# Performance work log

Hardware: AMD Instinct MI355X
Metric: run time of the kernel (lower is better)

Reference implementation:

```python
import jax, jax.numpy as jnp
import numpy as np


def setup_inputs() -> dict:
    key = jax.random.key(0)
    B, N = 4, 32768
    xyz = jax.random.normal(key, (B, N, 3), dtype=jnp.float32)
    return {"xyz": xyz, "K": 16, "nqueries": 2048}


def reference(xyz, K, nqueries):
    # xyz: (b, n, 3). Deterministic strided pick of nqueries query points
    # (stand-in for the KD-tree's distance-pick sampling), then brute-force KNN.
    b, n, _ = xyz.shape
    stride = n // nqueries
    q_idx = jnp.arange(nqueries) * stride          # (nq,)
    pts = xyz[:, q_idx, :]                          # (b, nq, 3) sampled query points
    # pairwise squared distances (b, nq, n)
    d = jnp.sum((pts[:, :, None, :] - xyz[:, None, :, :]) ** 2, axis=-1)
    _, idx = jax.lax.top_k(-d, K)                   # (b, nq, K) nearest-neighbor indices
    idx = idx.astype(jnp.int64)[..., None]          # (b, nq, K, 1) matches expand_dims(..., 3)
    return idx, pts
```

## Files before the change

### kernel.cpp

```cpp
#include <hip/hip_runtime.h>
#include <stdint.h>

#define NPTS  32768
#define NQ    2048
#define KNN   16
#define NB    4
#define BLOCK 256
#define WPB   4
#define PPL   8
#define ITERS (NPTS / (64 * PPL))
#define GATE_MARGIN 5e-4f

__device__ __forceinline__ int dpp_shr1_i(int x) {
    return __builtin_amdgcn_update_dpp(x, x, 0x111, 0xf, 0xf, false);
}
__device__ __forceinline__ float dpp_shr1_f(float x) {
    return __int_as_float(dpp_shr1_i(__float_as_int(x)));
}
__device__ __forceinline__ float readlane_f(float x, int l) {
    return __int_as_float(__builtin_amdgcn_readlane(__float_as_int(x), l));
}

template <int T>
__device__ __forceinline__ void insert_all(float d, int p, int lane,
                                           float& ld, int& li, float& tau,
                                           float& th, float qnm)
{
    unsigned long long rem = __ballot(d <= tau);
    while (rem) {
        const int srcl = __ffsll(rem) - 1;
        const float wd = readlane_f(d, srcl);
        const int   wi = __builtin_amdgcn_readlane(p, srcl);
        const bool less = (ld < wd) || (ld == wd && li < wi);
        const unsigned long long lm = __ballot(less);
        const int pos = __popc((unsigned)((lm >> (16 * T)) & 0xffffull));
        const float pld = dpp_shr1_f(ld);
        const int   pli = dpp_shr1_i(li);
        if ((lane >> 4) == T) {
            const int gl = lane & 15;
            if (gl == pos)      { ld = wd;  li = wi;  }
            else if (gl > pos)  { ld = pld; li = pli; }
        }
        tau = readlane_f(ld, 16 * T + 15);
        th  = tau + qnm;
        rem &= rem - 1;
        if (rem) rem &= __ballot(d <= tau);
    }
}

__device__ __forceinline__ void load6(float4 dst[6], const float4* p) {
    #pragma unroll
    for (int t = 0; t < 6; ++t) dst[t] = p[t];
}

__device__ __forceinline__ void step(const float4 c[6], int pb, int lane,
                                     float m2x0, float m2y0, float m2z0,
                                     float m2x1, float m2y1, float m2z1,
                                     float qx0, float qy0, float qz0,
                                     float qx1, float qy1, float qz1,
                                     float& ld, int& li,
                                     float& tau0, float& tau1,
                                     float& th0, float& th1,
                                     float qnm0, float qnm1)
{
    float px[PPL], py[PPL], pz[PPL];
    px[0] = c[0].x; py[0] = c[0].y; pz[0] = c[0].z;
    px[1] = c[0].w; py[1] = c[1].x; pz[1] = c[1].y;
    px[2] = c[1].z; py[2] = c[1].w; pz[2] = c[2].x;
    px[3] = c[2].y; py[3] = c[2].z; pz[3] = c[2].w;
    px[4] = c[3].x; py[4] = c[3].y; pz[4] = c[3].z;
    px[5] = c[3].w; py[5] = c[4].x; pz[5] = c[4].y;
    px[6] = c[4].z; py[6] = c[4].w; pz[6] = c[5].x;
    px[7] = c[5].y; py[7] = c[5].z; pz[7] = c[5].w;

    unsigned long long m0[PPL], m1[PPL], any = 0;
    #pragma unroll
    for (int j = 0; j < PPL; ++j) {
        const float s = __fmaf_rn(pz[j], pz[j],
                          __fmaf_rn(py[j], py[j], __fmul_rn(px[j], px[j])));
        float t0 = __fmaf_rn(px[j], m2x0, s);
        t0 = __fmaf_rn(py[j], m2y0, t0);
        t0 = __fmaf_rn(pz[j], m2z0, t0);
        m0[j] = __ballot(t0 <= th0);
        float t1 = __fmaf_rn(px[j], m2x1, s);
        t1 = __fmaf_rn(py[j], m2y1, t1);
        t1 = __fmaf_rn(pz[j], m2z1, t1);
        m1[j] = __ballot(t1 <= th1);
        any |= m0[j] | m1[j];
    }
    if (any) {
        #pragma unroll
        for (int j = 0; j < PPL; ++j) {
            if (m0[j]) {
                const float dx = __fadd_rn(px[j], -qx0);
                const float dy = __fadd_rn(py[j], -qy0);
                const float dz = __fadd_rn(pz[j], -qz0);
                const float d  = __fadd_rn(
                    __fadd_rn(__fmul_rn(dx, dx), __fmul_rn(dy, dy)),
                    __fmul_rn(dz, dz));
                insert_all<0>(d, pb + j, lane, ld, li, tau0, th0, qnm0);
            }
        }
        #pragma unroll
        for (int j = 0; j < PPL; ++j) {
            if (m1[j]) {
                const float dx = __fadd_rn(px[j], -qx1);
                const float dy = __fadd_rn(py[j], -qy1);
                const float dz = __fadd_rn(pz[j], -qz1);
                const float d  = __fadd_rn(
                    __fadd_rn(__fmul_rn(dx, dx), __fmul_rn(dy, dy)),
                    __fmul_rn(dz, dz));
                insert_all<1>(d, pb + j, lane, ld, li, tau1, th1, qnm1);
            }
        }
    }
}

__global__ __launch_bounds__(BLOCK) void knn_kernel(const float* __restrict__ xyz,
                                                    float* __restrict__ out_idx,
                                                    float* __restrict__ out_pts)
{
    const int tid  = threadIdx.x;
    const int lane = tid & 63;
    const int wv   = tid >> 6;
    const int w    = blockIdx.x * WPB + wv;
    const int b    = w >> 10;
    const int pr   = w & 1023;
    const size_t base = (size_t)b * NPTS * 3;

    const int qp0 = pr << 5;
    const float qx0 = xyz[base + 3 * qp0 + 0];
    const float qy0 = xyz[base + 3 * qp0 + 1];
    const float qz0 = xyz[base + 3 * qp0 + 2];
    const float qx1 = xyz[base + 3 * qp0 + 48];
    const float qy1 = xyz[base + 3 * qp0 + 49];
    const float qz1 = xyz[base + 3 * qp0 + 50];

    const int g0 = b * NQ + (pr << 1);
    if (lane == 0) {
        out_pts[3 * g0 + 0] = qx0;
        out_pts[3 * g0 + 1] = qy0;
        out_pts[3 * g0 + 2] = qz0;
        out_pts[3 * g0 + 3] = qx1;
        out_pts[3 * g0 + 4] = qy1;
        out_pts[3 * g0 + 5] = qz1;
    }

    const float m2x0 = -2.0f * qx0, m2y0 = -2.0f * qy0, m2z0 = -2.0f * qz0;
    const float m2x1 = -2.0f * qx1, m2y1 = -2.0f * qy1, m2z1 = -2.0f * qz1;
    const float qnm0 = -(qx0 * qx0 + qy0 * qy0 + qz0 * qz0) + GATE_MARGIN;
    const float qnm1 = -(qx1 * qx1 + qy1 * qy1 + qz1 * qz1) + GATE_MARGIN;

    float ld = __builtin_inff();  int li = 0x7fffffff;
    float tau0 = __builtin_inff(), tau1 = __builtin_inff();
    float th0  = __builtin_inff(), th1  = __builtin_inff();

    const float4* lp = (const float4*)(xyz + base) + 6 * lane;

    float4 A[6], Bf[6];
    load6(A, lp);
    for (int k = 0; k < ITERS; k += 2) {
        load6(Bf, lp + 384);
        step(A, (k << 9) + PPL * lane, lane,
             m2x0, m2y0, m2z0, m2x1, m2y1, m2z1,
             qx0, qy0, qz0, qx1, qy1, qz1,
             ld, li, tau0, tau1, th0, th1, qnm0, qnm1);
        if (k + 2 < ITERS)
            load6(A, lp + 768);
        step(Bf, ((k + 1) << 9) + PPL * lane, lane,
             m2x0, m2y0, m2z0, m2x1, m2y1, m2z1,
             qx0, qy0, qz0, qx1, qy1, qz1,
             ld, li, tau0, tau1, th0, th1, qnm0, qnm1);
        lp += 768;
    }

    if (lane < 2 * KNN) {
        out_idx[(size_t)g0 * KNN + lane] = (float)li;
    }
}

extern "C" void kernel_launch(void* const* d_in, const int* in_sizes, int n_in,
                              void* d_out, int out_size, void* d_ws, size_t ws_size,
                              hipStream_t stream) {
    const float* xyz = (const float*)d_in[0];
    float* out = (float*)d_out;
    float* out_idx = out;
    float* out_pts = out + (size_t)NB * NQ * KNN;

    const int blocks = (NB * NQ / 2) / WPB;
    knn_kernel<<<blocks, BLOCK, 0, stream>>>(xyz, out_idx, out_pts);
}
```

Measured before the change: 186.4 us.

## Repack points into float4 with precomputed norms and use one query per wave

Result: slower. 301.1 us (+61.5%).

```diff
diff --git a/kernel.cpp b/kernel.cpp
--- a/kernel.cpp
+++ b/kernel.cpp
@@ -5,10 +5,6 @@
 #define NQ    2048
 #define KNN   16
 #define NB    4
-#define BLOCK 256
-#define WPB   4
-#define PPL   8
-#define ITERS (NPTS / (64 * PPL))
 #define GATE_MARGIN 5e-4f
 
 __device__ __forceinline__ int dpp_shr1_i(int x) {
@@ -48,20 +44,133 @@
     }
 }
 
+__global__ __launch_bounds__(256) void repack_kernel(const float* __restrict__ xyz,
+                                                     float4* __restrict__ ws)
+{
+    const int i = blockIdx.x * 256 + threadIdx.x;
+    const float4* src = (const float4*)xyz + 3 * (size_t)i;
+    const float4 c0 = src[0], c1 = src[1], c2 = src[2];
+    float px[4], py[4], pz[4];
+    px[0] = c0.x; py[0] = c0.y; pz[0] = c0.z;
+    px[1] = c0.w; py[1] = c1.x; pz[1] = c1.y;
+    px[2] = c1.z; py[2] = c1.w; pz[2] = c2.x;
+    px[3] = c2.y; py[3] = c2.z; pz[3] = c2.w;
+    float4* dst = ws + 4 * (size_t)i;
+    #pragma unroll
+    for (int t = 0; t < 4; ++t) {
+        const float s = __fmaf_rn(pz[t], pz[t],
+                          __fmaf_rn(py[t], py[t], __fmul_rn(px[t], px[t])));
+        dst[t] = make_float4(px[t], py[t], pz[t], s);
+    }
+}
+
+#define BLOCKA 256
+#define WPBA   4
+#define PPLA   4
+#define ITERSA (NPTS / (64 * PPLA))
+
+__device__ __forceinline__ void load4(float4 dst[4], const float4* p) {
+    #pragma unroll
+    for (int t = 0; t < 4; ++t) dst[t] = p[t];
+}
+
+__device__ __forceinline__ void stepA(const float4 c[4], int pb, int lane,
+                                      float m2x, float m2y, float m2z,
+                                      float qx, float qy, float qz,
+                                      float& ld, int& li,
+                                      float& tau, float& th, float qnm)
+{
+    unsigned long long m[4], any = 0;
+    #pragma unroll
+    for (int j = 0; j < PPLA; ++j) {
+        float t = __fmaf_rn(c[j].x, m2x, c[j].w);
+        t = __fmaf_rn(c[j].y, m2y, t);
+        t = __fmaf_rn(c[j].z, m2z, t);
+        m[j] = __ballot(t <= th);
+        any |= m[j];
+    }
+    if (any) {
+        #pragma unroll
+        for (int j = 0; j < PPLA; ++j) {
+            if (m[j]) {
+                const float dx = __fadd_rn(c[j].x, -qx);
+                const float dy = __fadd_rn(c[j].y, -qy);
+                const float dz = __fadd_rn(c[j].z, -qz);
+                const float d  = __fadd_rn(
+                    __fadd_rn(__fmul_rn(dx, dx), __fmul_rn(dy, dy)),
+                    __fmul_rn(dz, dz));
+                insert_all<0>(d, pb + j, lane, ld, li, tau, th, qnm);
+            }
+        }
+    }
+}
+
+__global__ __launch_bounds__(BLOCKA) void knn1(const float4* __restrict__ wsp,
+                                               float* __restrict__ out_idx,
+                                               float* __restrict__ out_pts)
+{
+    const int tid  = threadIdx.x;
+    const int lane = tid & 63;
+    const int wv   = tid >> 6;
+    const int w    = blockIdx.x * WPBA + wv;
+    const int b    = w >> 11;
+    const int qi   = w & 2047;
+    const float4* pbase = wsp + (size_t)b * NPTS;
+
+    const float4 qv = pbase[qi << 4];
+    const float qx = qv.x, qy = qv.y, qz = qv.z;
+    const float m2x = -2.0f * qx, m2y = -2.0f * qy, m2z = -2.0f * qz;
+    const float qnm = -qv.w + GATE_MARGIN;
+
+    const int g = b * NQ + qi;
+    if (lane == 0) {
+        out_pts[3 * g + 0] = qx;
+        out_pts[3 * g + 1] = qy;
+        out_pts[3 * g + 2] = qz;
+    }
+
+    float ld = __builtin_inff();  int li = 0x7fffffff;
+    float tau = __builtin_inff(), th = __builtin_inff();
+
+    const float4* lp = pbase + 4 * lane;
+
+    float4 A[4], Bf[4];
+    load4(A, lp);
+    for (int k = 0; k < ITERSA; k += 2) {
+        load4(Bf, lp + 256);
+        stepA(A, (k << 8) + 4 * lane, lane, m2x, m2y, m2z,
+              qx, qy, qz, ld, li, tau, th, qnm);
+        if (k + 2 < ITERSA)
+            load4(A, lp + 512);
+        stepA(Bf, ((k + 1) << 8) + 4 * lane, lane, m2x, m2y, m2z,
+              qx, qy, qz, ld, li, tau, th, qnm);
+        lp += 512;
+    }
+
+    if (lane < KNN) {
+        out_idx[(size_t)g * KNN + lane] = (float)li;
+    }
+}
+
+#define BLOCK 256
+#define WPB   4
+#define PPL   8
+#define ITERS (NPTS / (64 * PPL))
+
 __device__ __forceinline__ void load6(float4 dst[6], const float4* p) {
     #pragma unroll
     for (int t = 0; t < 6; ++t) dst[t] = p[t];
 }
 
-__device__ __forceinline__ void step(const float4 c[6], int pb, int lane,
-                                     float m2x0, float m2y0, float m2z0,
-                                     float m2x1, float m2y1, float m2z1,
-                                     float qx0, float qy0, float qz0,
-                                     float qx1, float qy1, float qz1,
-                                     float& ld, int& li,
-                                     float& tau0, float& tau1,
-                                     float& th0, float& th1,
-                                     float qnm0, float qnm1)
+__device__ __forceinline__ void step2(const float4 c[6], int pb, int lane,
+                                      float m2x0, float m2y0, float m2z0,
+                                      float m2x1, float m2y1, float m2z1,
+                                      float qx0, float qy0, float qz0,
+                                      float qx1, float qy1, float qz1,
+                                      float& ld, int& li,
+                                      float& tau0, float& tau1,
+                                      float& th0, float& th1,
+                                      float qnm0, float qnm1)
 {
     float px[PPL], py[PPL], pz[PPL];
     px[0] = c[0].x; py[0] = c[0].y; pz[0] = c[0].z;
@@ -116,9 +225,9 @@
     }
 }
 
-__global__ __launch_bounds__(BLOCK) void knn_kernel(const float* __restrict__ xyz,
-                                                    float* __restrict__ out_idx,
-                                                    float* __restrict__ out_pts)
+__global__ __launch_bounds__(BLOCK) void knn2(const float* __restrict__ xyz,
+                                              float* __restrict__ out_idx,
+                                              float* __restrict__ out_pts)
 {
     const int tid  = threadIdx.x;
     const int lane = tid & 63;
@@ -161,16 +270,16 @@
     load6(A, lp);
     for (int k = 0; k < ITERS; k += 2) {
         load6(Bf, lp + 384);
-        step(A, (k << 9) + PPL * lane, lane,
-             m2x0, m2y0, m2z0, m2x1, m2y1, m2z1,
-             qx0, qy0, qz0, qx1, qy1, qz1,
-             ld, li, tau0, tau1, th0, th1, qnm0, qnm1);
+        step2(A, (k << 9) + PPL * lane, lane,
+              m2x0, m2y0, m2z0, m2x1, m2y1, m2z1,
+              qx0, qy0, qz0, qx1, qy1, qz1,
+              ld, li, tau0, tau1, th0, th1, qnm0, qnm1);
         if (k + 2 < ITERS)
             load6(A, lp + 768);
-        step(Bf, ((k + 1) << 9) + PPL * lane, lane,
-             m2x0, m2y0, m2z0, m2x1, m2y1, m2z1,
-             qx0, qy0, qz0, qx1, qy1, qz1,
-             ld, li, tau0, tau1, th0, th1, qnm0, qnm1);
+        step2(Bf, ((k + 1) << 9) + PPL * lane, lane,
+              m2x0, m2y0, m2z0, m2x1, m2y1, m2z1,
+              qx0, qy0, qz0, qx1, qy1, qz1,
+              ld, li, tau0, tau1, th0, th1, qnm0, qnm1);
         lp += 768;
     }
 
@@ -187,6 +296,12 @@
     float* out_idx = out;
     float* out_pts = out + (size_t)NB * NQ * KNN;
 
-    const int blocks = (NB * NQ / 2) / WPB;
-    knn_kernel<<<blocks, BLOCK, 0, stream>>>(xyz, out_idx, out_pts);
-}
+    const size_t ws_needed = (size_t)NB * NPTS * sizeof(float4);
+    if (d_ws != nullptr && ws_size >= ws_needed) {
+        float4* wsp = (float4*)d_ws;
+        repack_kernel<<<NB * NPTS / (4 * 256), 256, 0, stream>>>(xyz, wsp);
+        knn1<<<NB * NQ / WPBA, BLOCKA, 0, stream>>>(wsp, out_idx, out_pts);
+    } else {
+        knn2<<<(NB * NQ / 2) / WPB, BLOCK, 0, stream>>>(xyz, out_idx, out_pts);
+    }
+}
```

## Repack points to SoA in workspace and use packed FP32 math for gating

Applied to the files above, without the earlier changes.

Result: no change. 185.1 us (-0.7%).

```diff
diff --git a/kernel.cpp b/kernel.cpp
--- a/kernel.cpp
+++ b/kernel.cpp
@@ -11,6 +11,8 @@
 #define ITERS (NPTS / (64 * PPL))
 #define GATE_MARGIN 5e-4f
 
+typedef float f32x2 __attribute__((ext_vector_type(2)));
+
 __device__ __forceinline__ int dpp_shr1_i(int x) {
     return __builtin_amdgcn_update_dpp(x, x, 0x111, 0xf, 0xf, false);
 }
@@ -19,6 +21,17 @@
 }
 __device__ __forceinline__ float readlane_f(float x, int l) {
     return __int_as_float(__builtin_amdgcn_readlane(__float_as_int(x), l));
+}
+
+__device__ __forceinline__ f32x2 pk_mul(f32x2 a, f32x2 b) {
+    f32x2 d;
+    asm("v_pk_mul_f32 %0, %1, %2" : "=v"(d) : "v"(a), "v"(b));
+    return d;
+}
+__device__ __forceinline__ f32x2 pk_fma(f32x2 a, f32x2 b, f32x2 c) {
+    f32x2 d;
+    asm("v_pk_fma_f32 %0, %1, %2, %3" : "=v"(d) : "v"(a), "v"(b), "v"(c));
+    return d;
 }
 
 template <int T>
@@ -48,20 +61,175 @@
     }
 }
 
+__global__ __launch_bounds__(256) void repack_soa(const float* __restrict__ xyz,
+                                                  float* __restrict__ ws)
+{
+    const int i = blockIdx.x * 256 + threadIdx.x;
+    const int b = i / (NPTS / 4);
+    const int g = i % (NPTS / 4);
+    const float4* src = (const float4*)(xyz + (size_t)b * NPTS * 3) + 3 * g;
+    const float4 c0 = src[0], c1 = src[1], c2 = src[2];
+    float* xs = ws + (size_t)b * 3 * NPTS;
+    float* ys = xs + NPTS;
+    float* zs = ys + NPTS;
+    ((float4*)xs)[g] = make_float4(c0.x, c0.w, c1.z, c2.y);
+    ((float4*)ys)[g] = make_float4(c0.y, c1.x, c1.w, c2.z);
+    ((float4*)zs)[g] = make_float4(c0.z, c1.y, c2.x, c2.w);
+}
+
+struct PtBuf { float4 x0, x1, y0, y1, z0, z1; };
+
+__device__ __forceinline__ void loadbuf(PtBuf& b, const float* xs,
+                                        const float* ys, const float* zs,
+                                        unsigned o)
+{
+    b.x0 = *(const float4*)(xs + o);  b.x1 = *(const float4*)(xs + o + 4);
+    b.y0 = *(const float4*)(ys + o);  b.y1 = *(const float4*)(ys + o + 4);
+    b.z0 = *(const float4*)(zs + o);  b.z1 = *(const float4*)(zs + o + 4);
+}
+
+__device__ __forceinline__ void step_soa(const PtBuf& c, int pb, int lane,
+                                         f32x2 M2X0, f32x2 M2Y0, f32x2 M2Z0,
+                                         f32x2 M2X1, f32x2 M2Y1, f32x2 M2Z1,
+                                         float qx0, float qy0, float qz0,
+                                         float qx1, float qy1, float qz1,
+                                         float& ld, int& li,
+                                         float& tau0, float& tau1,
+                                         float& th0, float& th1,
+                                         float qnm0, float qnm1)
+{
+    f32x2 X[4] = { {c.x0.x, c.x0.y}, {c.x0.z, c.x0.w},
+                   {c.x1.x, c.x1.y}, {c.x1.z, c.x1.w} };
+    f32x2 Y[4] = { {c.y0.x, c.y0.y}, {c.y0.z, c.y0.w},
+                   {c.y1.x, c.y1.y}, {c.y1.z, c.y1.w} };
+    f32x2 Z[4] = { {c.z0.x, c.z0.y}, {c.z0.z, c.z0.w},
+                   {c.z1.x, c.z1.y}, {c.z1.z, c.z1.w} };
+
+    unsigned long long m0[PPL], m1[PPL], any = 0;
+    #pragma unroll
+    for (int u = 0; u < 4; ++u) {
+        const f32x2 s  = pk_fma(Z[u], Z[u], pk_fma(Y[u], Y[u], pk_mul(X[u], X[u])));
+        const f32x2 t0 = pk_fma(Z[u], M2Z0, pk_fma(Y[u], M2Y0, pk_fma(X[u], M2X0, s)));
+        const f32x2 t1 = pk_fma(Z[u], M2Z1, pk_fma(Y[u], M2Y1, pk_fma(X[u], M2X1, s)));
+        m0[2*u]   = __ballot(t0.x <= th0);
+        m0[2*u+1] = __ballot(t0.y <= th0);
+        m1[2*u]   = __ballot(t1.x <= th1);
+        m1[2*u+1] = __ballot(t1.y <= th1);
+        any |= m0[2*u] | m0[2*u+1] | m1[2*u] | m1[2*u+1];
+    }
+    if (any) {
+        #pragma unroll
+        for (int j = 0; j < PPL; ++j) {
+            if (m0[j]) {
+                const float pxj = (j & 1) ? X[j >> 1].y : X[j >> 1].x;
+                const float pyj = (j & 1) ? Y[j >> 1].y : Y[j >> 1].x;
+                const float pzj = (j & 1) ? Z[j >> 1].y : Z[j >> 1].x;
+                const float dx = __fadd_rn(pxj, -qx0);
+                const float dy = __fadd_rn(pyj, -qy0);
+                const float dz = __fadd_rn(pzj, -qz0);
+                const float d  = __fadd_rn(
+                    __fadd_rn(__fmul_rn(dx, dx), __fmul_rn(dy, dy)),
+                    __fmul_rn(dz, dz));
+                insert_all<0>(d, pb + j, lane, ld, li, tau0, th0, qnm0);
+            }
+        }
+        #pragma unroll
+        for (int j = 0; j < PPL; ++j) {
+            if (m1[j]) {
+                const float pxj = (j & 1) ? X[j >> 1].y : X[j >> 1].x;
+                const float pyj = (j & 1) ? Y[j >> 1].y : Y[j >> 1].x;
+                const float pzj = (j & 1) ? Z[j >> 1].y : Z[j >> 1].x;
+                const float dx = __fadd_rn(pxj, -qx1);
+                const float dy = __fadd_rn(pyj, -qy1);
+                const float dz = __fadd_rn(pzj, -qz1);
+                const float d  = __fadd_rn(
+                    __fadd_rn(__fmul_rn(dx, dx), __fmul_rn(dy, dy)),
+                    __fmul_rn(dz, dz));
+                insert_all<1>(d, pb + j, lane, ld, li, tau1, th1, qnm1);
+            }
+        }
+    }
+}
+
+__global__ __launch_bounds__(BLOCK) void knn_soa(const float* __restrict__ ws,
+                                                 float* __restrict__ out_idx,
+                                                 float* __restrict__ out_pts)
+{
+    const int tid  = threadIdx.x;
+    const int lane = tid & 63;
+    const int wv   = tid >> 6;
+    const int w    = blockIdx.x * WPB + wv;
+    const int b    = w >> 10;
+    const int pr   = w & 1023;
+    const float* xs = ws + (size_t)b * 3 * NPTS;
+    const float* ys = xs + NPTS;
+    const float* zs = ys + NPTS;
+
+    const int qp0 = pr << 5;
+    const float qx0 = xs[qp0],      qy0 = ys[qp0],      qz0 = zs[qp0];
+    const float qx1 = xs[qp0 + 16], qy1 = ys[qp0 + 16], qz1 = zs[qp0 + 16];
+
+    const int g0 = b * NQ + (pr << 1);
+    if (lane == 0) {
+        out_pts[3 * g0 + 0] = qx0;
+        out_pts[3 * g0 + 1] = qy0;
+        out_pts[3 * g0 + 2] = qz0;
+        out_pts[3 * g0 + 3] = qx1;
+        out_pts[3 * g0 + 4] = qy1;
+        out_pts[3 * g0 + 5] = qz1;
+    }
+
+    const f32x2 M2X0 = { -2.0f * qx0, -2.0f * qx0 };
+    const f32x2 M2Y0 = { -2.0f * qy0, -2.0f * qy0 };
+    const f32x2 M2Z0 = { -2.0f * qz0, -2.0f * qz0 };
+    const f32x2 M2X1 = { -2.0f * qx1, -2.0f * qx1 };
+    const f32x2 M2Y1 = { -2.0f * qy1, -2.0f * qy1 };
+    const f32x2 M2Z1 = { -2.0f * qz1, -2.0f * qz1 };
+    const float qnm0 = -(qx0 * qx0 + qy0 * qy0 + qz0 * qz0) + GATE_MARGIN;
+    const float qnm1 = -(qx1 * qx1 + qy1 * qy1 + qz1 * qz1) + GATE_MARGIN;
+
+    float ld = __builtin_inff();  int li = 0x7fffffff;
+    float tau0 = __builtin_inff(), tau1 = __builtin_inff();
+    float th0  = __builtin_inff(), th1  = __builtin_inff();
+
+    unsigned o = 8 * (unsigned)lane;
+
+    PtBuf A, Bf;
+    loadbuf(A, xs, ys, zs, o);
+    int pb = PPL * lane;
+    for (int k = 0; k < ITERS; k += 2) {
+        loadbuf(Bf, xs, ys, zs, o + 512);
+        step_soa(A, pb, lane, M2X0, M2Y0, M2Z0, M2X1, M2Y1, M2Z1,
+                 qx0, qy0, qz0, qx1, qy1, qz1,
+                 ld, li, tau0, tau1, th0, th1, qnm0, qnm1);
+        if (k + 2 < ITERS)
+            loadbuf(A, xs, ys, zs, o + 1024);
+        step_soa(Bf, pb + 512, lane, M2X0, M2Y0, M2Z0, M2X1, M2Y1, M2Z1,
+                 qx0, qy0, qz0, qx1, qy1, qz1,
+                 ld, li, tau0, tau1, th0, th1, qnm0, qnm1);
+        o += 1024;
+        pb += 1024;
+    }
+
+    if (lane < 2 * KNN) {
+        out_idx[(size_t)g0 * KNN + lane] = (float)li;
+    }
+}
+
 __device__ __forceinline__ void load6(float4 dst[6], const float4* p) {
     #pragma unroll
     for (int t = 0; t < 6; ++t) dst[t] = p[t];
 }
 
-__device__ __forceinline__ void step(const float4 c[6], int pb, int lane,
-                                     float m2x0, float m2y0, float m2z0,
-                                     float m2x1, float m2y1, float m2z1,
-                                     float qx0, float qy0, float qz0,
-                                     float qx1, float qy1, float qz1,
-                                     float& ld, int& li,
-                                     float& tau0, float& tau1,
-                                     float& th0, float& th1,
-                                     float qnm0, float qnm1)
+__device__ __forceinline__ void step2(const float4 c[6], int pb, int lane,
+                                      float m2x0, float m2y0, float m2z0,
+                                      float m2x1, float m2y1, float m2z1,
+                                      float qx0, float qy0, float qz0,
+                                      float qx1, float qy1, float qz1,
+                                      float& ld, int& li,
+                                      float& tau0, float& tau1,
+                                      float& th0, float& th1,
+                                      float qnm0, float qnm1)
 {
     float px[PPL], py[PPL], pz[PPL];
     px[0] = c[0].x; py[0] = c[0].y; pz[0] = c[0].z;
@@ -116,9 +284,9 @@
     }
 }
 
-__global__ __launch_bounds__(BLOCK) void knn_kernel(const float* __restrict__ xyz,
-                                                    float* __restrict__ out_idx,
-                                                    float* __restrict__ out_pts)
+__global__ __launch_bounds__(BLOCK) void knn_aos(const float* __restrict__ xyz,
+                                                 float* __restrict__ out_idx,
+                                                 float* __restrict__ out_pts)
 {
     const int tid  = threadIdx.x;
     const int lane = tid & 63;
@@ -161,16 +329,16 @@
     load6(A, lp);
     for (int k = 0; k < ITERS; k += 2) {
         load6(Bf, lp + 384);
-        step(A, (k << 9) + PPL * lane, lane,
-             m2x0, m2y0, m2z0, m2x1, m2y1, m2z1,
-             qx0, qy0, qz0, qx1, qy1, qz1,
-             ld, li, tau0, tau1, th0, th1, qnm0, qnm1);
+        step2(A, (k << 9) + PPL * lane, lane,
+              m2x0, m2y0, m2z0, m2x1, m2y1, m2z1,
+              qx0, qy0, qz0, qx1, qy1, qz1,
+              ld, li, tau0, tau1, th0, th1, qnm0, qnm1);
         if (k + 2 < ITERS)
             load6(A, lp + 768);
-        step(Bf, ((k + 1) << 9) + PPL * lane, lane,
-             m2x0, m2y0, m2z0, m2x1, m2y1, m2z1,
-             qx0, qy0, qz0, qx1, qy1, qz1,
-             ld, li, tau0, tau1, th0, th1, qnm0, qnm1);
+        step2(Bf, ((k + 1) << 9) + PPL * lane, lane,
+              m2x0, m2y0, m2z0, m2x1, m2y1, m2z1,
+              qx0, qy0, qz0, qx1, qy1, qz1,
+              ld, li, tau0, tau1, th0, th1, qnm0, qnm1);
         lp += 768;
     }
 
@@ -187,6 +355,13 @@
     float* out_idx = out;
     float* out_pts = out + (size_t)NB * NQ * KNN;
 
+    const size_t ws_needed = (size_t)NB * 3 * NPTS * sizeof(float);
     const int blocks = (NB * NQ / 2) / WPB;
-    knn_kernel<<<blocks, BLOCK, 0, stream>>>(xyz, out_idx, out_pts);
-}
+    if (d_ws != nullptr && ws_size >= ws_needed) {
+        float* wsp = (float*)d_ws;
+        repack_soa<<<NB * NPTS / 4 / 256, 256, 0, stream>>>(xyz, wsp);
+        knn_soa<<<blocks, BLOCK, 0, stream>>>(wsp, out_idx, out_pts);
+    } else {
+        knn_aos<<<blocks, BLOCK, 0, stream>>>(xyz, out_idx, out_pts);
+    }
+}
```
